# Performance work log

Measured on AMD Instinct MI355X. Metric: run time of the kernel, lower is better.

Reference implementation:

```python
import jax, jax.numpy as jnp
import numpy as np

NUM_NODES = 10000  # fixed by input spec: edge_index values in [0, 10000)


def setup_inputs() -> dict:
    key = jax.random.key(0)
    k1, k2, k3 = jax.random.split(key, 3)
    N, E, D_IN, D_OUT = NUM_NODES, 320000, 256, 256
    x = jax.random.normal(k1, (N, D_IN), dtype=jnp.float32)
    edge_index = jax.random.randint(k2, (2, E), 0, N, dtype=jnp.int64)
    # ensure node N-1 appears so num_nodes == N as in the torch code
    edge_index = edge_index.at[0, 0].set(N - 1)
    # xavier_uniform for [D_IN, D_OUT]
    limit = float(np.sqrt(6.0 / (D_IN + D_OUT)))
    weight = jax.random.uniform(k3, (D_IN, D_OUT), dtype=jnp.float32,
                                minval=-limit, maxval=limit)
    return {"x": x, "edge_index": edge_index, "weight": weight}


def _normalize_adjacency(edge_index, num_nodes):
    src, dst = edge_index[0], edge_index[1]
    ones = jnp.ones(src.shape[0], dtype=jnp.float32)
    # symmetric binarized adjacency: adj[i,j] = adj[j,i] = 1 (set, not add)
    adj = jnp.zeros((num_nodes, num_nodes), dtype=jnp.float32)
    adj = adj.at[src, dst].max(ones)
    adj = adj.at[dst, src].max(ones)
    # one round of self-loops: adj += I
    adj = adj + jnp.eye(num_nodes, dtype=jnp.float32)
    deg = jnp.sum(adj, axis=1)                    # [N]
    dinv = 1.0 / jnp.sqrt(deg)                    # [N]
    # D^-1/2 A D^-1/2 via broadcasting (equivalent to diag mms)
    return adj * dinv[:, None] * dinv[None, :]


def reference(x, edge_index, weight):
    adj = _normalize_adjacency(edge_index, NUM_NODES)  # [N, N]
    h = adj @ x                                        # [N, D_IN]
    return h @ weight                                  # [N, D_OUT]
```

## Files before the change

kernel.cpp:

```cpp
#include <hip/hip_runtime.h>
#include <hip/hip_bf16.h>
#include <stdint.h>

#define N_NODES   10000
#define D_FEAT    256
#define E_EDGES   320000
#define ROW_WORDS 313

#define NB     625
#define RPB    16
#define B_CAP  1536
#define NBLK_E 313
#define NBLK_G 625
#define NBLK_C 625
#define COLSTR 128

#define LDSTR 264

typedef __attribute__((ext_vector_type(4))) float float4v;
typedef _Float16 half8  __attribute__((ext_vector_type(8)));
typedef _Float16 half4v __attribute__((ext_vector_type(4)));

__device__ __forceinline__ float h2f_lo(uint32_t u) {
    union { uint32_t u; _Float16 h[2]; } v; v.u = u; return (float)v.h[0];
}
__device__ __forceinline__ float h2f_hi(uint32_t u) {
    union { uint32_t u; _Float16 h[2]; } v; v.u = u; return (float)v.h[1];
}


__global__ void __launch_bounds__(1024)
wcast_k(const float* __restrict__ w, _Float16* __restrict__ wt,
        uint32_t* __restrict__ cursors) {
    __shared__ float st[1024];
    int t = threadIdx.x;
    if (blockIdx.x == 0) cursors[t] = 0u;
    int kb = blockIdx.x * 4;
    int k = kb + (t >> 8), n = t & 255;
    st[(n << 2) | (t >> 8)] = w[(size_t)k * D_FEAT + n];
    __syncthreads();
    if (t < 256) {
        half4v o = { (_Float16)st[t * 4 + 0], (_Float16)st[t * 4 + 1],
                     (_Float16)st[t * 4 + 2], (_Float16)st[t * 4 + 3] };
        *(half4v*)&wt[(size_t)t * D_FEAT + kb] = o;
    }
}

__global__ void __launch_bounds__(1024)
sort_gemm(const int* __restrict__ ei, uint32_t* __restrict__ bucketbuf,
          uint32_t* __restrict__ cursors,
          const float* __restrict__ x, const _Float16* __restrict__ wt,
          _Float16* __restrict__ yw) {
    __shared__ __align__(16) uint8_t smraw[24640];
    int t = threadIdx.x;
    int wv = t >> 6, lane = t & 63;

    if (blockIdx.x >= NBLK_E) {
        _Float16* a_lds = (_Float16*)smraw;
        int r0 = (blockIdx.x - NBLK_E) * 16;
        int row = t >> 6, c4 = (t & 63) * 4;
        float4v xv = *(const float4v*)(x + (size_t)(r0 + row) * D_FEAT + c4);
        half4v h = { (_Float16)xv[0], (_Float16)xv[1],
                     (_Float16)xv[2], (_Float16)xv[3] };
        *(half4v*)&a_lds[row * LDSTR + c4] = h;
        __syncthreads();
        int quad = lane >> 4, r = lane & 15;
        int ct = wv;
        const _Float16* pb = wt + (size_t)(ct * 16 + r) * D_FEAT + quad * 8;
        float4v acc = {0.f, 0.f, 0.f, 0.f};
        #pragma unroll
        for (int kk = 0; kk < D_FEAT; kk += 32) {
            half8 a = *(const half8*)&a_lds[r * LDSTR + kk + quad * 8];
            half8 b = *(const half8*)(pb + kk);
            acc = __builtin_amdgcn_mfma_f32_16x16x32_f16(a, b, acc, 0, 0, 0);
        }
        int colg = ct * 16 + r;
        #pragma unroll
        for (int u = 0; u < 4; u++)
            yw[(size_t)(r0 + quad * 4 + u) * D_FEAT + colg] = (_Float16)acc[u];
        return;
    }

    uint32_t* hist   = (uint32_t*)(smraw);
    uint32_t* lofs   = (uint32_t*)(smraw + 4096);
    uint32_t* base_s = (uint32_t*)(smraw + 8192);
    uint32_t* wsum   = (uint32_t*)(smraw + 12288);
    uint32_t* stage  = (uint32_t*)(smraw + 12352);
    uint16_t* sbkt   = (uint16_t*)(smraw + 20544);

    hist[t] = 0;
    __syncthreads();
    int e = blockIdx.x * 1024 + t;
    int b0 = -1, b1 = -1; uint32_t ent0 = 0, ent1 = 0, s0 = 0, s1 = 0;
    if (e < E_EDGES) {
        int s = ei[e], d = ei[E_EDGES + e];
        if ((uint32_t)s < N_NODES && (uint32_t)d < N_NODES) {
            b0 = s >> 4; ent0 = ((uint32_t)(s & 15) << 14) | (uint32_t)d;
            b1 = d >> 4; ent1 = ((uint32_t)(d & 15) << 14) | (uint32_t)s;
            s0 = atomicAdd(&hist[b0], 1u);
            s1 = atomicAdd(&hist[b1], 1u);
        }
    }
    __syncthreads();
    uint32_t h = hist[t];
    uint32_t incl = h;
    #pragma unroll
    for (int off = 1; off < 64; off <<= 1) {
        uint32_t v = __shfl_up(incl, off, 64);
        if (lane >= off) incl += v;
    }
    if (lane == 63) wsum[wv] = incl;
    __syncthreads();
    if (wv == 0) {
        uint32_t s = (lane < 16) ? wsum[lane] : 0u;
        #pragma unroll
        for (int off = 1; off < 16; off <<= 1) {
            uint32_t v = __shfl_up(s, off, 64);
            if (lane >= off) s += v;
        }
        if (lane < 16) wsum[lane] = s;
    }
    __syncthreads();
    uint32_t wbase = wv ? wsum[wv - 1] : 0u;
    lofs[t] = incl + wbase;
    base_s[t] = h ? atomicAdd(&cursors[t], h) : 0u;
    __syncthreads();
    if (b0 >= 0) {
        uint32_t p0 = lofs[b0] - hist[b0] + s0;
        stage[p0] = ent0; sbkt[p0] = (uint16_t)b0;
        uint32_t p1 = lofs[b1] - hist[b1] + s1;
        stage[p1] = ent1; sbkt[p1] = (uint16_t)b1;
    }
    __syncthreads();
    uint32_t total = lofs[1023];
    for (uint32_t idx = t; idx < total; idx += 1024) {
        uint32_t b = sbkt[idx];
        uint32_t pos = base_s[b] + (idx - (lofs[b] - hist[b]));
        if (pos < B_CAP) bucketbuf[(size_t)b * B_CAP + pos] = stage[idx];
    }
}

__global__ void __launch_bounds__(1024)
csr_only(const uint32_t* __restrict__ bucketbuf, const uint32_t* __restrict__ cursors,
         uint32_t* __restrict__ row_deg, float* __restrict__ dinv,
         uint16_t* __restrict__ col) {
    __shared__ __align__(16) uint32_t bm[RPB * ROW_WORDS];
    int t = threadIdx.x;
    int b = blockIdx.x;
    for (int i = t; i < RPB * ROW_WORDS; i += 1024) bm[i] = 0;
    __syncthreads();
    uint32_t cnt = min(cursors[b], (uint32_t)B_CAP);
    const uint32_t* bb = bucketbuf + (size_t)b * B_CAP;
    for (uint32_t i = t; i < cnt; i += 1024) {
        uint32_t ent = bb[i];
        uint32_t lr = ent >> 14, d = ent & 0x3FFFu;
        atomicOr(&bm[lr * ROW_WORDS + (d >> 5)], 1u << (d & 31));
    }
    __syncthreads();
    int wv = t >> 6, lane = t & 63;
    {
        int r = wv;
        int gi = b * RPB + r;
        uint32_t wb[5]; int tot = 0;
        #pragma unroll
        for (int k = 0; k < 5; k++) {
            int w = lane + 64 * k;
            uint32_t v = (w < ROW_WORDS) ? bm[r * ROW_WORDS + w] : 0u;
            wb[k] = v; tot += __popc(v);
        }
        int incl = tot;
        #pragma unroll
        for (int off = 1; off < 64; off <<= 1) {
            int v = __shfl_up(incl, off, 64);
            if (lane >= off) incl += v;
        }
        uint32_t total = (uint32_t)__shfl(incl, 63, 64);
        if (lane == 0) {
            row_deg[gi] = min(total, (uint32_t)COLSTR);
            dinv[gi]    = 1.0f / sqrtf((float)(total + 1u));
        }
        uint32_t p = (uint32_t)(incl - tot);
        #pragma unroll
        for (int k = 0; k < 5; k++) {
            uint32_t bits = wb[k];
            uint32_t cbase = (uint32_t)(lane + 64 * k) << 5;
            while (bits) {
                if (p < COLSTR)
                    col[(size_t)gi * COLSTR + p] =
                        (uint16_t)(cbase + (uint32_t)__builtin_ctz(bits));
                p++;
                bits &= bits - 1;
            }
        }
    }
}

__global__ void __launch_bounds__(256)
spmm_out(const uint32_t* __restrict__ row_deg, const float* __restrict__ dinv,
         const uint16_t* __restrict__ col, const _Float16* __restrict__ ywp,
         float* __restrict__ out) {
    const uint16_t* yw = (const uint16_t*)ywp;
    int wv = threadIdx.x >> 6, lane = threadIdx.x & 63;
    int half = lane >> 5, sl = lane & 31;
    int i = blockIdx.x * 4 + wv;
    uint32_t base = (uint32_t)i * COLSTR;
    uint32_t deg = min(row_deg[i], (uint32_t)COLSTR);
    float di = dinv[i];
    size_t ch = (size_t)sl * 8;
    float4v z = {0.f, 0.f, 0.f, 0.f};
    float4v accl[8], acch[8];
    #pragma unroll
    for (int k = 0; k < 8; k++) { accl[k] = z; acch[k] = z; }

    uint32_t hb = (uint32_t)(half << 3);
    uint4 cv = {0u, 0u, 0u, 0u};
    if (deg) cv = *(const uint4*)&col[base + hb];

    for (uint32_t t = 0; t < deg; t += 16) {
        uint4 cvn = {0u, 0u, 0u, 0u};
        uint32_t tn = t + 16;
        if (tn < deg) cvn = *(const uint4*)&col[base + tn + hb];
        uint32_t tb = t + hb;
        uint32_t jr[8];
        jr[0] = cv.x & 0xffffu; jr[1] = cv.x >> 16;
        jr[2] = cv.y & 0xffffu; jr[3] = cv.y >> 16;
        jr[4] = cv.z & 0xffffu; jr[5] = cv.z >> 16;
        jr[6] = cv.w & 0xffffu; jr[7] = cv.w >> 16;
        uint4 g[8]; float dk[8];
        #pragma unroll
        for (int k = 0; k < 8; k++) {
            uint32_t j = min(jr[k], (uint32_t)(N_NODES - 1));
            g[k]  = *(const uint4*)(yw + ((size_t)j << 8) + ch);
            dk[k] = dinv[j];
        }
        #pragma unroll
        for (int k = 0; k < 8; k++) {
            float d = (tb + (uint32_t)k < deg) ? dk[k] : 0.f;
            accl[k][0] += d * h2f_lo(g[k].x); accl[k][1] += d * h2f_hi(g[k].x);
            accl[k][2] += d * h2f_lo(g[k].y); accl[k][3] += d * h2f_hi(g[k].y);
            acch[k][0] += d * h2f_lo(g[k].z); acch[k][1] += d * h2f_hi(g[k].z);
            acch[k][2] += d * h2f_lo(g[k].w); acch[k][3] += d * h2f_hi(g[k].w);
        }
        cv = cvn;
    }

    if (half == 0) {
        const uint4 gs = *(const uint4*)(yw + ((size_t)i << 8) + ch);
        accl[0][0] += di * h2f_lo(gs.x); accl[0][1] += di * h2f_hi(gs.x);
        accl[0][2] += di * h2f_lo(gs.y); accl[0][3] += di * h2f_hi(gs.y);
        acch[0][0] += di * h2f_lo(gs.z); acch[0][1] += di * h2f_hi(gs.z);
        acch[0][2] += di * h2f_lo(gs.w); acch[0][3] += di * h2f_hi(gs.w);
    }

    float4v lo = ((accl[0] + accl[1]) + (accl[2] + accl[3])) +
                 ((accl[4] + accl[5]) + (accl[6] + accl[7]));
    float4v hi = ((acch[0] + acch[1]) + (acch[2] + acch[3])) +
                 ((acch[4] + acch[5]) + (acch[6] + acch[7]));
    #pragma unroll
    for (int u = 0; u < 4; u++) {
        lo[u] += __shfl_xor(lo[u], 32, 64);
        hi[u] += __shfl_xor(hi[u], 32, 64);
    }
    float4v res;
    if (half) res = hi; else res = lo;
    float* op = out + (size_t)i * D_FEAT + (size_t)sl * 8 + (half ? 4 : 0);
    *(float4v*)op = di * res;
}

extern "C" void kernel_launch(void* const* d_in, const int* in_sizes, int n_in,
                              void* d_out, int out_size, void* d_ws, size_t ws_size,
                              hipStream_t stream) {
    const float* x  = (const float*)d_in[0];
    const int*   ei = (const int*)d_in[1];
    const float* w  = (const float*)d_in[2];
    float* out = (float*)d_out;
    uint8_t* ws = (uint8_t*)d_ws;

    const size_t BB_OFF   = 4096;
    const size_t RD_OFF   = 3844096;
    const size_t DI_OFF   = 3884096;
    const size_t WT_OFF   = 3924096;
    const size_t YW_OFF   = 4055168;
    const size_t COL_OFF  = 9175168;
    const size_t NEED     = 11735168;

    if (ws_size < NEED) return;

    uint32_t* cursors   = (uint32_t*)ws;
    uint32_t* bucketbuf = (uint32_t*)(ws + BB_OFF);
    uint32_t* row_deg   = (uint32_t*)(ws + RD_OFF);
    float*    dinv      = (float*)(ws + DI_OFF);
    _Float16* wt        = (_Float16*)(ws + WT_OFF);
    _Float16* yw        = (_Float16*)(ws + YW_OFF);
    uint16_t* col       = (uint16_t*)(ws + COL_OFF);

    wcast_k  <<<64, 1024, 0, stream>>>(w, wt, cursors);
    sort_gemm<<<NBLK_E + NBLK_G, 1024, 0, stream>>>(ei, bucketbuf, cursors,
                                                    x, wt, yw);
    csr_only <<<NBLK_C, 1024, 0, stream>>>(bucketbuf, cursors,
                                           row_deg, dinv, col);
    spmm_out <<<N_NODES / 4, 256, 0, stream>>>(row_deg, dinv, col, yw, out);
}
```

Measured before the change: 129.5 us.

## Split SpMM feature dimension across two blocks and vectorize bitmap zeroing

The SpMM kernel now launches twice as many blocks, and each block handles one 128-column half of the feature row. Each lane gathers 8-byte chunks instead of 16 bytes, which halves the accumulator registers and should raise occupancy and memory-level parallelism. The cost is that column indices and dinv are read twice per row, gathers become narrower, and half the lanes sit idle at the store. Separately, the shared bitmap in csr_only is zeroed with 16-byte stores.

```diff
diff --git a/kernel.cpp b/kernel.cpp
--- a/kernel.cpp
+++ b/kernel.cpp
@@ -147,7 +147,11 @@
     __shared__ __align__(16) uint32_t bm[RPB * ROW_WORDS];
     int t = threadIdx.x;
     int b = blockIdx.x;
-    for (int i = t; i < RPB * ROW_WORDS; i += 1024) bm[i] = 0;
+    {
+        uint4 zz = {0u, 0u, 0u, 0u};
+        uint4* bm4 = (uint4*)bm;
+        for (int i = t; i < (RPB * ROW_WORDS) / 4; i += 1024) bm4[i] = zz;
+    }
     __syncthreads();
     uint32_t cnt = min(cursors[b], (uint32_t)B_CAP);
     const uint32_t* bb = bucketbuf + (size_t)b * B_CAP;
@@ -196,23 +200,25 @@
 }
 
 __global__ void __launch_bounds__(256)
-spmm_out(const uint32_t* __restrict__ row_deg, const float* __restrict__ dinv,
-         const uint16_t* __restrict__ col, const _Float16* __restrict__ ywp,
-         float* __restrict__ out) {
+spmm_half(const uint32_t* __restrict__ row_deg, const float* __restrict__ dinv,
+          const uint16_t* __restrict__ col, const _Float16* __restrict__ ywp,
+          float* __restrict__ out) {
     const uint16_t* yw = (const uint16_t*)ywp;
+    int bid = blockIdx.x;
+    int h = bid & 1;
     int wv = threadIdx.x >> 6, lane = threadIdx.x & 63;
-    int half = lane >> 5, sl = lane & 31;
-    int i = blockIdx.x * 4 + wv;
+    int hw = lane >> 5, sl = lane & 31;
+    int i = (bid >> 1) * 4 + wv;
     uint32_t base = (uint32_t)i * COLSTR;
     uint32_t deg = min(row_deg[i], (uint32_t)COLSTR);
     float di = dinv[i];
-    size_t ch = (size_t)sl * 8;
+    size_t ch = (size_t)(h << 7) + (size_t)sl * 4;
     float4v z = {0.f, 0.f, 0.f, 0.f};
-    float4v accl[8], acch[8];
+    float4v a[8];
     #pragma unroll
-    for (int k = 0; k < 8; k++) { accl[k] = z; acch[k] = z; }
-
-    uint32_t hb = (uint32_t)(half << 3);
+    for (int k = 0; k < 8; k++) a[k] = z;
+
+    uint32_t hb = (uint32_t)(hw << 3);
     uint4 cv = {0u, 0u, 0u, 0u};
     if (deg) cv = *(const uint4*)&col[base + hb];
 
@@ -226,45 +232,36 @@
         jr[2] = cv.y & 0xffffu; jr[3] = cv.y >> 16;
         jr[4] = cv.z & 0xffffu; jr[5] = cv.z >> 16;
         jr[6] = cv.w & 0xffffu; jr[7] = cv.w >> 16;
-        uint4 g[8]; float dk[8];
+        uint2 g[8]; float dk[8];
         #pragma unroll
         for (int k = 0; k < 8; k++) {
             uint32_t j = min(jr[k], (uint32_t)(N_NODES - 1));
-            g[k]  = *(const uint4*)(yw + ((size_t)j << 8) + ch);
+            g[k]  = *(const uint2*)(yw + ((size_t)j << 8) + ch);
             dk[k] = dinv[j];
         }
         #pragma unroll
         for (int k = 0; k < 8; k++) {
             float d = (tb + (uint32_t)k < deg) ? dk[k] : 0.f;
-            accl[k][0] += d * h2f_lo(g[k].x); accl[k][1] += d * h2f_hi(g[k].x);
-            accl[k][2] += d * h2f_lo(g[k].y); accl[k][3] += d * h2f_hi(g[k].y);
-            acch[k][0] += d * h2f_lo(g[k].z); acch[k][1] += d * h2f_hi(g[k].z);
-            acch[k][2] += d * h2f_lo(g[k].w); acch[k][3] += d * h2f_hi(g[k].w);
+            a[k][0] += d * h2f_lo(g[k].x); a[k][1] += d * h2f_hi(g[k].x);
+            a[k][2] += d * h2f_lo(g[k].y); a[k][3] += d * h2f_hi(g[k].y);
         }
         cv = cvn;
     }
 
-    if (half == 0) {
-        const uint4 gs = *(const uint4*)(yw + ((size_t)i << 8) + ch);
-        accl[0][0] += di * h2f_lo(gs.x); accl[0][1] += di * h2f_hi(gs.x);
-        accl[0][2] += di * h2f_lo(gs.y); accl[0][3] += di * h2f_hi(gs.y);
-        acch[0][0] += di * h2f_lo(gs.z); acch[0][1] += di * h2f_hi(gs.z);
-        acch[0][2] += di * h2f_lo(gs.w); acch[0][3] += di * h2f_hi(gs.w);
-    }
-
-    float4v lo = ((accl[0] + accl[1]) + (accl[2] + accl[3])) +
-                 ((accl[4] + accl[5]) + (accl[6] + accl[7]));
-    float4v hi = ((acch[0] + acch[1]) + (acch[2] + acch[3])) +
-                 ((acch[4] + acch[5]) + (acch[6] + acch[7]));
+    if (hw == 0) {
+        const uint2 gs = *(const uint2*)(yw + ((size_t)i << 8) + ch);
+        a[0][0] += di * h2f_lo(gs.x); a[0][1] += di * h2f_hi(gs.x);
+        a[0][2] += di * h2f_lo(gs.y); a[0][3] += di * h2f_hi(gs.y);
+    }
+
+    float4v acc = ((a[0] + a[1]) + (a[2] + a[3])) + ((a[4] + a[5]) + (a[6] + a[7]));
     #pragma unroll
-    for (int u = 0; u < 4; u++) {
-        lo[u] += __shfl_xor(lo[u], 32, 64);
-        hi[u] += __shfl_xor(hi[u], 32, 64);
-    }
-    float4v res;
-    if (half) res = hi; else res = lo;
-    float* op = out + (size_t)i * D_FEAT + (size_t)sl * 8 + (half ? 4 : 0);
-    *(float4v*)op = di * res;
+    for (int u = 0; u < 4; u++)
+        acc[u] += __shfl_xor(acc[u], 32, 64);
+    if (hw == 0) {
+        float* op = out + (size_t)i * D_FEAT + (h << 7) + sl * 4;
+        *(float4v*)op = di * acc;
+    }
 }
 
 extern "C" void kernel_launch(void* const* d_in, const int* in_sizes, int n_in,
@@ -299,5 +296,5 @@
                                                     x, wt, yw);
     csr_only <<<NBLK_C, 1024, 0, stream>>>(bucketbuf, cursors,
                                            row_deg, dinv, col);
-    spmm_out <<<N_NODES / 4, 256, 0, stream>>>(row_deg, dinv, col, yw, out);
-}
+    spmm_half<<<N_NODES / 2, 256, 0, stream>>>(row_deg, dinv, col, yw, out);
+}
```

New measurement: 129.4 us. Within noise of the previous version (-0.1%).
